# Kernel optimization log

Measured on AMD Instinct MI355X. Metric: run time of the kernel, lower is better.

The kernel has to match this reference:

```python
import jax, jax.numpy as jnp
import numpy as np

N, E, IN, H = 20000, 50000, 32, 64


def _lin_init(k, fan_in, shape):
    b = 1.0 / np.sqrt(fan_in)
    return jax.random.uniform(k, shape, jnp.float32, -b, b)


def setup_inputs() -> dict:
    key = jax.random.key(0)
    ks = jax.random.split(key, 16)
    inp = {
        "x": jax.random.normal(ks[0], (N, IN), jnp.float32),
        "edge_index": jax.random.randint(ks[1], (2, E), 0, N, dtype=jnp.int32),
        "edge_attr": jax.random.normal(ks[2], (E, 1, 2), jnp.float32),
        # layer 0: edge MLP 2->H->IN*H, root [IN,H], bias [H]
        "w1_0": _lin_init(ks[3], 2, (2, H)),
        "b1_0": _lin_init(ks[4], 2, (H,)),
        "w2_0": _lin_init(ks[5], H, (H, IN * H)),
        "b2_0": _lin_init(ks[6], H, (IN * H,)),
        "root_0": _lin_init(ks[7], IN, (IN, H)),
        "bias_0": _lin_init(ks[8], IN, (H,)),
        # layer 1: edge MLP 2->H->H*H, root [H,H], bias [H]
        "w1_1": _lin_init(ks[9], 2, (2, H)),
        "b1_1": _lin_init(ks[10], 2, (H,)),
        "w2_1": _lin_init(ks[11], H, (H, H * H)),
        "b2_1": _lin_init(ks[12], H, (H * H,)),
        "root_1": _lin_init(ks[13], H, (H, H)),
        "bias_1": _lin_init(ks[14], H, (H,)),
    }
    return inp


def _nnconv(x, src, dst, ea, w1, b1, w2, b2, root, bias, in_c, out_c):
    # per-edge weight matrices from edge-attr MLP: [E, in_c*out_c]
    h = jax.nn.relu(ea @ w1 + b1) @ w2 + b2
    W = h.reshape(-1, in_c, out_c)                     # [E, in, out]
    msg = jnp.einsum('ei,eio->eo', x[src], W)          # gather + per-edge matmul
    agg = jax.ops.segment_sum(msg, dst, num_segments=x.shape[0])  # scatter-add
    return agg + x @ root + bias                       # add aggr (PyG NNConv, aggr='add')


def reference(x, edge_index, edge_attr,
              w1_0, b1_0, w2_0, b2_0, root_0, bias_0,
              w1_1, b1_1, w2_1, b2_1, root_1, bias_1):
    src, dst = edge_index[0], edge_index[1]
    ea = edge_attr.reshape(edge_attr.shape[0], 2)      # [E, 2]
    x = jax.nn.relu(_nnconv(x, src, dst, ea, w1_0, b1_0, w2_0, b2_0, root_0, bias_0, IN, H))
    x = jax.nn.relu(_nnconv(x, src, dst, ea, w1_1, b1_1, w2_1, b2_1, root_1, bias_1, H, H))
    return x
```

## Files before the change

### kernel.cpp

```cpp
#include <hip/hip_runtime.h>

typedef _Float16 v8h __attribute__((ext_vector_type(8)));
typedef float v16f __attribute__((ext_vector_type(16)));

#define NBF0 (68 * 2 * 2 * 512)
#define NBF1 (68 * 4 * 2 * 512)

__global__ void prep_bf_both(const float* __restrict__ w2_0, const float* __restrict__ b2_0,
                             _Float16* __restrict__ BF0,
                             const float* __restrict__ w2_1, const float* __restrict__ b2_1,
                             _Float16* __restrict__ BF1) {
    int idx = blockIdx.x * 256 + threadIdx.x;
    if (idx < NBF0) {
        int rel = idx;
        int j = rel & 7, lane = (rel >> 3) & 63, f = rel >> 9;
        int nf = f & 1, kk16 = f >> 1;
        int k = kk16 * 16 + (lane >> 5) * 8 + j;
        int ko = k >> 5, i = k & 31;
        int o = nf * 32 + (lane & 31);
        float v = (ko < 64) ? w2_0[ko * (32 * 64) + i * 64 + o]
                : (ko == 64 ? b2_0[i * 64 + o] : 0.f);
        BF0[rel] = (_Float16)v;
    } else if (idx < NBF0 + NBF1) {
        int rel = idx - NBF0;
        int j = rel & 7, lane = (rel >> 3) & 63, f = rel >> 9;
        int nf = f & 1, kk16 = f >> 1;
        int k = kk16 * 16 + (lane >> 5) * 8 + j;
        int ko = k >> 6, i = k & 63;
        int o = nf * 32 + (lane & 31);
        float v = (ko < 64) ? w2_1[ko * (64 * 64) + i * 64 + o]
                : (ko == 64 ? b2_1[i * 64 + o] : 0.f);
        BF1[rel] = (_Float16)v;
    }
}

__global__ void node_root_cvt(const float* __restrict__ x, const float* __restrict__ root,
                              const float* __restrict__ bias, float* __restrict__ agg,
                              _Float16* __restrict__ xb, int N) {
    int idx = blockIdx.x * 256 + threadIdx.x;
    if (idx >= N * 64) return;
    int n = idx >> 6, o = idx & 63;
    float s = bias[o];
    const float* xr = x + (size_t)n * 32;
    #pragma unroll 8
    for (int i = 0; i < 32; ++i) s += xr[i] * root[i * 64 + o];
    agg[idx] = s;
    if (o < 32) xb[n * 32 + o] = (_Float16)xr[o];
}

__global__ void mid_kernel(const float* __restrict__ agg0, const float* __restrict__ root1,
                           const float* __restrict__ bias1, _Float16* __restrict__ x1b,
                           float* __restrict__ agg1, int N) {
    int idx = blockIdx.x * 256 + threadIdx.x;
    if (idx >= N * 64) return;
    int n = idx >> 6, o = idx & 63;
    const float* ar = agg0 + (size_t)n * 64;
    float s = bias1[o];
    #pragma unroll 8
    for (int i = 0; i < 64; ++i) s += fmaxf(ar[i], 0.f) * root1[i * 64 + o];
    agg1[idx] = s;
    x1b[idx] = (_Float16)fmaxf(agg0[idx], 0.f);
}

__global__ void final_relu(const float* __restrict__ agg1, float* __restrict__ out, int n) {
    int idx = blockIdx.x * 256 + threadIdx.x;
    if (idx < n) out[idx] = fmaxf(agg1[idx], 0.f);
}

template<int IN_C>
__global__ __launch_bounds__(256) __attribute__((amdgpu_waves_per_eu(3, 3)))
void edge_gemm(const float* __restrict__ ea,
               const float* __restrict__ w1, const float* __restrict__ b1v,
               const _Float16* __restrict__ xb, const _Float16* __restrict__ BF,
               const int* __restrict__ srcI, const int* __restrict__ dstI,
               float* __restrict__ agg, int E) {
    constexpr int PH  = IN_C / 16;
    constexpr int CPR = IN_C / 8;

    __shared__ __align__(16) _Float16 sh_x[64][IN_C];
    __shared__ _Float16 sh_r1[64][70];
    __shared__ float buf[64][65];
    __shared__ int sh_dst[64];

    int tid = threadIdx.x;
    int ebase = blockIdx.x * 64;
    int valid = E - ebase; if (valid > 64) valid = 64;

    if (tid < 64) {
        sh_dst[tid] = (tid < valid) ? dstI[ebase + tid] : 0;
        sh_r1[tid][64] = (_Float16)1.f;
        #pragma unroll
        for (int c = 65; c < 70; ++c) sh_r1[tid][c] = (_Float16)0.f;
    }
    for (int i = tid; i < 64 * 64; i += 256) {
        int e = i >> 6, j = i & 63;
        int ge = (e < valid) ? (ebase + e) : ebase;
        float a0 = ea[ge * 2], a1 = ea[ge * 2 + 1];
        sh_r1[e][j] = (_Float16)fmaxf(a0 * w1[j] + a1 * w1[64 + j] + b1v[j], 0.f);
    }
    for (int i = tid; i < 64 * CPR; i += 256) {
        int r = i / CPR, c = i - r * CPR;
        int sidx = (r < valid) ? srcI[ebase + r] : 0;
        *(uint4*)&sh_x[r][c * 8] = *(const uint4*)(xb + (size_t)sidx * IN_C + (size_t)c * 8);
    }
    __syncthreads();

    int wv = tid >> 6, lane = tid & 63, ln = lane & 31, g2 = lane >> 5;
    int nf = wv & 1, kh = wv >> 1;

    v8h xs0[PH], xs1[PH];
    #pragma unroll
    for (int p = 0; p < PH; ++p) {
        xs0[p] = *(const v8h*)&sh_x[ln][p * 16 + g2 * 8];
        xs1[p] = *(const v8h*)&sh_x[ln + 32][p * 16 + g2 * 8];
    }

    v16f acc0 = {0,0,0,0,0,0,0,0,0,0,0,0,0,0,0,0};
    v16f acc1 = acc0;

    const uint4* bp = (const uint4*)BF + (size_t)nf * 64 + lane;
    int kb = kh * 33;

    uint4 pb0[PH], pb1[PH], pb2[PH];
    auto LD = [&](uint4 (&d)[PH], int ko) {
        #pragma unroll
        for (int p = 0; p < PH; ++p) d[p] = bp[(size_t)(ko * PH + p) * 128];
    };
    auto FM = [&](uint4 (&d)[PH], int ko) {
        _Float16 sv0 = sh_r1[ln][ko];
        _Float16 sv1 = sh_r1[ln + 32][ko];
        #pragma unroll
        for (int p = 0; p < PH; ++p) {
            v8h bb; __builtin_memcpy(&bb, &d[p], 16);
            v8h a0 = xs0[p] * sv0;
            v8h a1 = xs1[p] * sv1;
            acc0 = __builtin_amdgcn_mfma_f32_32x32x16_f16(a0, bb, acc0, 0, 0, 0);
            acc1 = __builtin_amdgcn_mfma_f32_32x32x16_f16(a1, bb, acc1, 0, 0, 0);
        }
    };

    LD(pb0, kb);
    LD(pb1, kb + 1);
    #pragma unroll 1
    for (int t = 0; t < 11; ++t) {
        int base = kb + 3 * t;
        LD(pb2, base + 2);
        FM(pb0, base);
        LD(pb0, base + 3);
        FM(pb1, base + 1);
        LD(pb1, base + 4);
        FM(pb2, base + 2);
    }

    int colb = nf * 32 + ln;
    if (kh == 1) {
        #pragma unroll
        for (int r = 0; r < 16; ++r) {
            int row = 4 * g2 + (r & 3) + 8 * (r >> 2);
            buf[row][colb]      = acc0[r];
            buf[row + 32][colb] = acc1[r];
        }
    }
    __syncthreads();
    if (kh == 0) {
        #pragma unroll
        for (int r = 0; r < 16; ++r) {
            int row = 4 * g2 + (r & 3) + 8 * (r >> 2);
            if (row < valid)
                atomicAdd(&agg[(size_t)sh_dst[row] * 64 + colb], acc0[r] + buf[row][colb]);
            int row1 = row + 32;
            if (row1 < valid)
                atomicAdd(&agg[(size_t)sh_dst[row1] * 64 + colb], acc1[r] + buf[row1][colb]);
        }
    }
}

extern "C" void kernel_launch(void* const* d_in, const int* in_sizes, int n_in,
                              void* d_out, int out_size, void* d_ws, size_t ws_size,
                              hipStream_t stream) {
    const float* x      = (const float*)d_in[0];
    const int*   ei     = (const int*)d_in[1];
    const float* ea     = (const float*)d_in[2];
    const float* w1_0   = (const float*)d_in[3];
    const float* b1_0   = (const float*)d_in[4];
    const float* w2_0   = (const float*)d_in[5];
    const float* b2_0   = (const float*)d_in[6];
    const float* root_0 = (const float*)d_in[7];
    const float* bias_0 = (const float*)d_in[8];
    const float* w1_1   = (const float*)d_in[9];
    const float* b1_1   = (const float*)d_in[10];
    const float* w2_1   = (const float*)d_in[11];
    const float* b2_1   = (const float*)d_in[12];
    const float* root_1 = (const float*)d_in[13];
    const float* bias_1 = (const float*)d_in[14];
    float* out = (float*)d_out;

    int N = in_sizes[0] / 32;
    int E = in_sizes[1] / 2;
    const int* srcI = ei;
    const int* dstI = ei + E;

    char* ws = (char*)d_ws;
    size_t off = 0;
    auto carve = [&](size_t bytes) {
        void* p = ws + off;
        off += (bytes + 255) & ~(size_t)255;
        return p;
    };
    _Float16* BF0  = (_Float16*)carve((size_t)NBF0 * 2);
    _Float16* BF1  = (_Float16*)carve((size_t)NBF1 * 2);
    _Float16* XB0  = (_Float16*)carve((size_t)N * 32 * 2);
    _Float16* X1B  = (_Float16*)carve((size_t)N * 64 * 2);
    float*    AGG0 = (float*)carve((size_t)N * 64 * 4);
    float*    AGG1 = (float*)carve((size_t)N * 64 * 4);

    int tbf = NBF0 + NBF1;
    prep_bf_both<<<(tbf + 255) / 256, 256, 0, stream>>>(w2_0, b2_0, BF0, w2_1, b2_1, BF1);
    node_root_cvt<<<(N * 64 + 255) / 256, 256, 0, stream>>>(x, root_0, bias_0, AGG0, XB0, N);

    int gblocks = (E + 63) / 64;
    edge_gemm<32><<<gblocks, 256, 0, stream>>>(ea, w1_0, b1_0, XB0, BF0, srcI, dstI, AGG0, E);

    mid_kernel<<<(N * 64 + 255) / 256, 256, 0, stream>>>(AGG0, root_1, bias_1, X1B, AGG1, N);

    edge_gemm<64><<<gblocks, 256, 0, stream>>>(ea, w1_1, b1_1, X1B, BF1, srcI, dstI, AGG1, E);

    final_relu<<<(N * 64 + 255) / 256, 256, 0, stream>>>(AGG1, out, N * 64);
}
```

Measured before the change: 191.7 us.

## Split K dimension four ways per wave and reduce via shared-memory atomics

Each of the four waves now computes the full 64x64 output tile over a quarter of the K range (17 outer steps), reusing each A fragment across both N halves with four accumulators. Partial results are combined with LDS atomicAdd into a zeroed buffer, then all threads issue coalesced global atomics. This removes the redundant A-operand scaling per N half and the manual triple-buffered prefetch pipeline. In exchange it costs extra accumulator registers, LDS atomic contention, and the loss of explicit load/compute overlap.

```diff
diff --git a/kernel.cpp b/kernel.cpp
--- a/kernel.cpp
+++ b/kernel.cpp
@@ -78,7 +78,7 @@
     constexpr int CPR = IN_C / 8;
 
     __shared__ __align__(16) _Float16 sh_x[64][IN_C];
-    __shared__ _Float16 sh_r1[64][70];
+    __shared__ _Float16 sh_r1[64][72];
     __shared__ float buf[64][65];
     __shared__ int sh_dst[64];
 
@@ -90,7 +90,7 @@
         sh_dst[tid] = (tid < valid) ? dstI[ebase + tid] : 0;
         sh_r1[tid][64] = (_Float16)1.f;
         #pragma unroll
-        for (int c = 65; c < 70; ++c) sh_r1[tid][c] = (_Float16)0.f;
+        for (int c = 65; c < 72; ++c) sh_r1[tid][c] = (_Float16)0.f;
     }
     for (int i = tid; i < 64 * 64; i += 256) {
         int e = i >> 6, j = i & 63;
@@ -103,10 +103,13 @@
         int sidx = (r < valid) ? srcI[ebase + r] : 0;
         *(uint4*)&sh_x[r][c * 8] = *(const uint4*)(xb + (size_t)sidx * IN_C + (size_t)c * 8);
     }
+    {
+        float* bf = &buf[0][0];
+        for (int i = tid; i < 64 * 65; i += 256) bf[i] = 0.f;
+    }
     __syncthreads();
 
     int wv = tid >> 6, lane = tid & 63, ln = lane & 31, g2 = lane >> 5;
-    int nf = wv & 1, kh = wv >> 1;
 
     v8h xs0[PH], xs1[PH];
     #pragma unroll
@@ -115,63 +118,51 @@
         xs1[p] = *(const v8h*)&sh_x[ln + 32][p * 16 + g2 * 8];
     }
 
-    v16f acc0 = {0,0,0,0,0,0,0,0,0,0,0,0,0,0,0,0};
-    v16f acc1 = acc0;
-
-    const uint4* bp = (const uint4*)BF + (size_t)nf * 64 + lane;
-    int kb = kh * 33;
-
-    uint4 pb0[PH], pb1[PH], pb2[PH];
-    auto LD = [&](uint4 (&d)[PH], int ko) {
-        #pragma unroll
-        for (int p = 0; p < PH; ++p) d[p] = bp[(size_t)(ko * PH + p) * 128];
-    };
-    auto FM = [&](uint4 (&d)[PH], int ko) {
+    v16f acc00 = {0,0,0,0,0,0,0,0,0,0,0,0,0,0,0,0};
+    v16f acc01 = acc00, acc10 = acc00, acc11 = acc00;
+
+    const uint4* bp = (const uint4*)BF + lane;
+    int kb = wv * 17;
+
+    for (int ko = kb; ko < kb + 17; ++ko) {
+        uint4 b0[PH], b1[PH];
+        #pragma unroll
+        for (int p = 0; p < PH; ++p) {
+            size_t f2 = (size_t)(ko * PH + p) * 2;
+            b0[p] = bp[f2 * 64];
+            b1[p] = bp[(f2 + 1) * 64];
+        }
         _Float16 sv0 = sh_r1[ln][ko];
         _Float16 sv1 = sh_r1[ln + 32][ko];
         #pragma unroll
         for (int p = 0; p < PH; ++p) {
-            v8h bb; __builtin_memcpy(&bb, &d[p], 16);
+            v8h bb0; __builtin_memcpy(&bb0, &b0[p], 16);
+            v8h bb1; __builtin_memcpy(&bb1, &b1[p], 16);
             v8h a0 = xs0[p] * sv0;
             v8h a1 = xs1[p] * sv1;
-            acc0 = __builtin_amdgcn_mfma_f32_32x32x16_f16(a0, bb, acc0, 0, 0, 0);
-            acc1 = __builtin_amdgcn_mfma_f32_32x32x16_f16(a1, bb, acc1, 0, 0, 0);
+            acc00 = __builtin_amdgcn_mfma_f32_32x32x16_f16(a0, bb0, acc00, 0, 0, 0);
+            acc01 = __builtin_amdgcn_mfma_f32_32x32x16_f16(a0, bb1, acc01, 0, 0, 0);
+            acc10 = __builtin_amdgcn_mfma_f32_32x32x16_f16(a1, bb0, acc10, 0, 0, 0);
+            acc11 = __builtin_amdgcn_mfma_f32_32x32x16_f16(a1, bb1, acc11, 0, 0, 0);
+        }
+    }
+
+    auto emit = [&](const v16f& c, int mf, int nf) {
+        int col = nf * 32 + ln;
+        #pragma unroll
+        for (int r = 0; r < 16; ++r) {
+            int row = mf * 32 + 4 * g2 + (r & 3) + 8 * (r >> 2);
+            atomicAdd(&buf[row][col], c[r]);
         }
     };
-
-    LD(pb0, kb);
-    LD(pb1, kb + 1);
-    #pragma unroll 1
-    for (int t = 0; t < 11; ++t) {
-        int base = kb + 3 * t;
-        LD(pb2, base + 2);
-        FM(pb0, base);
-        LD(pb0, base + 3);
-        FM(pb1, base + 1);
-        LD(pb1, base + 4);
-        FM(pb2, base + 2);
-    }
-
-    int colb = nf * 32 + ln;
-    if (kh == 1) {
-        #pragma unroll
-        for (int r = 0; r < 16; ++r) {
-            int row = 4 * g2 + (r & 3) + 8 * (r >> 2);
-            buf[row][colb]      = acc0[r];
-            buf[row + 32][colb] = acc1[r];
-        }
-    }
+    emit(acc00, 0, 0); emit(acc01, 0, 1);
+    emit(acc10, 1, 0); emit(acc11, 1, 1);
     __syncthreads();
-    if (kh == 0) {
-        #pragma unroll
-        for (int r = 0; r < 16; ++r) {
-            int row = 4 * g2 + (r & 3) + 8 * (r >> 2);
-            if (row < valid)
-                atomicAdd(&agg[(size_t)sh_dst[row] * 64 + colb], acc0[r] + buf[row][colb]);
-            int row1 = row + 32;
-            if (row1 < valid)
-                atomicAdd(&agg[(size_t)sh_dst[row1] * 64 + colb], acc1[r] + buf[row1][colb]);
-        }
+
+    for (int t = tid; t < 64 * 64; t += 256) {
+        int row = t >> 6, col = t & 63;
+        if (row < valid)
+            atomicAdd(&agg[(size_t)sh_dst[row] * 64 + col], buf[row][col]);
     }
 }
 
```

New measurement: 347.2 us. 81.1% more time.

## Stage edge-MLP weight fragments in LDS via async loads, split K across grid

Applied to the files above, without the earlier changes.

Each block now covers 128 edges instead of 64. The K dimension (hidden units plus the bias row) is split across a second grid dimension, so every block handles 34 K-steps for all 128 edges. Weight fragments are copied into a double-buffered LDS area with global_load_lds and shared by the two 64-edge wave groups, where before each wave read them straight from global memory. This halves the weight traffic per edge and drops the in-block cross-wave reduction buffer. The costs are a __syncthreads on every K-step, twice as many atomicAdds (one per K-half) and the removed waves_per_eu hint.

```diff
diff --git a/kernel.cpp b/kernel.cpp
--- a/kernel.cpp
+++ b/kernel.cpp
@@ -68,110 +68,96 @@
 }
 
 template<int IN_C>
-__global__ __launch_bounds__(256) __attribute__((amdgpu_waves_per_eu(3, 3)))
+__global__ __launch_bounds__(256)
 void edge_gemm(const float* __restrict__ ea,
                const float* __restrict__ w1, const float* __restrict__ b1v,
                const _Float16* __restrict__ xb, const _Float16* __restrict__ BF,
                const int* __restrict__ srcI, const int* __restrict__ dstI,
                float* __restrict__ agg, int E) {
-    constexpr int PH  = IN_C / 16;
-    constexpr int CPR = IN_C / 8;
-
-    __shared__ __align__(16) _Float16 sh_x[64][IN_C];
-    __shared__ _Float16 sh_r1[64][70];
-    __shared__ float buf[64][65];
-    __shared__ int sh_dst[64];
+    constexpr int PH    = IN_C / 16;
+    constexpr int NB_FR = PH * 2;
+    constexpr int CPR   = IN_C / 8;
+    constexpr int KO_B  = 34;
+
+    __shared__ __align__(16) _Float16 sh_b[2][NB_FR * 512];
+    __shared__ __align__(16) _Float16 sh_x[128][IN_C];
+    __shared__ _Float16 sh_r1[128][36];
+    __shared__ int sh_dst[128];
 
     int tid = threadIdx.x;
-    int ebase = blockIdx.x * 64;
-    int valid = E - ebase; if (valid > 64) valid = 64;
-
-    if (tid < 64) {
-        sh_dst[tid] = (tid < valid) ? dstI[ebase + tid] : 0;
-        sh_r1[tid][64] = (_Float16)1.f;
-        #pragma unroll
-        for (int c = 65; c < 70; ++c) sh_r1[tid][c] = (_Float16)0.f;
-    }
-    for (int i = tid; i < 64 * 64; i += 256) {
-        int e = i >> 6, j = i & 63;
+    int ebase = blockIdx.x * 128;
+    int kb = blockIdx.y * KO_B;
+    int valid = E - ebase; if (valid > 128) valid = 128;
+
+    if (tid < 128) sh_dst[tid] = (tid < valid) ? dstI[ebase + tid] : 0;
+
+    for (int i = tid; i < 128 * 36; i += 256) {
+        int e = i / 36, jj = i - e * 36;
+        int j = kb + jj;
         int ge = (e < valid) ? (ebase + e) : ebase;
-        float a0 = ea[ge * 2], a1 = ea[ge * 2 + 1];
-        sh_r1[e][j] = (_Float16)fmaxf(a0 * w1[j] + a1 * w1[64 + j] + b1v[j], 0.f);
-    }
-    for (int i = tid; i < 64 * CPR; i += 256) {
+        float v;
+        if (j < 64)       v = fmaxf(ea[ge * 2] * w1[j] + ea[ge * 2 + 1] * w1[64 + j] + b1v[j], 0.f);
+        else if (j == 64) v = 1.f;
+        else              v = 0.f;
+        sh_r1[e][jj] = (_Float16)v;
+    }
+    for (int i = tid; i < 128 * CPR; i += 256) {
         int r = i / CPR, c = i - r * CPR;
         int sidx = (r < valid) ? srcI[ebase + r] : 0;
         *(uint4*)&sh_x[r][c * 8] = *(const uint4*)(xb + (size_t)sidx * IN_C + (size_t)c * 8);
     }
+
+    int wv = tid >> 6, lane = tid & 63, ln = lane & 31, g2 = lane >> 5;
+    int nf = wv & 1, eg = wv >> 1;
+
+    auto stage = [&](int c, int buf) {
+        const _Float16* g = BF + (size_t)(kb + c) * (NB_FR * 512);
+        for (int q = wv; q < NB_FR; q += 4) {
+            __builtin_amdgcn_global_load_lds(
+                (const __attribute__((address_space(1))) void*)(g + q * 512 + lane * 8),
+                (__attribute__((address_space(3))) void*)(&sh_b[buf][q * 512]),
+                16, 0, 0);
+        }
+    };
+
+    stage(0, 0);
     __syncthreads();
-
-    int wv = tid >> 6, lane = tid & 63, ln = lane & 31, g2 = lane >> 5;
-    int nf = wv & 1, kh = wv >> 1;
 
     v8h xs0[PH], xs1[PH];
     #pragma unroll
     for (int p = 0; p < PH; ++p) {
-        xs0[p] = *(const v8h*)&sh_x[ln][p * 16 + g2 * 8];
-        xs1[p] = *(const v8h*)&sh_x[ln + 32][p * 16 + g2 * 8];
+        xs0[p] = *(const v8h*)&sh_x[eg * 64 + ln][p * 16 + g2 * 8];
+        xs1[p] = *(const v8h*)&sh_x[eg * 64 + 32 + ln][p * 16 + g2 * 8];
     }
 
     v16f acc0 = {0,0,0,0,0,0,0,0,0,0,0,0,0,0,0,0};
     v16f acc1 = acc0;
 
-    const uint4* bp = (const uint4*)BF + (size_t)nf * 64 + lane;
-    int kb = kh * 33;
-
-    uint4 pb0[PH], pb1[PH], pb2[PH];
-    auto LD = [&](uint4 (&d)[PH], int ko) {
-        #pragma unroll
-        for (int p = 0; p < PH; ++p) d[p] = bp[(size_t)(ko * PH + p) * 128];
-    };
-    auto FM = [&](uint4 (&d)[PH], int ko) {
-        _Float16 sv0 = sh_r1[ln][ko];
-        _Float16 sv1 = sh_r1[ln + 32][ko];
+    for (int c = 0; c < KO_B; ++c) {
+        if (c + 1 < KO_B) stage(c + 1, (c + 1) & 1);
+        const _Float16* bb = sh_b[c & 1];
+        _Float16 sv0 = sh_r1[eg * 64 + ln][c];
+        _Float16 sv1 = sh_r1[eg * 64 + 32 + ln][c];
         #pragma unroll
         for (int p = 0; p < PH; ++p) {
-            v8h bb; __builtin_memcpy(&bb, &d[p], 16);
+            v8h bf = *(const v8h*)(bb + (p * 2 + nf) * 512 + lane * 8);
             v8h a0 = xs0[p] * sv0;
             v8h a1 = xs1[p] * sv1;
-            acc0 = __builtin_amdgcn_mfma_f32_32x32x16_f16(a0, bb, acc0, 0, 0, 0);
-            acc1 = __builtin_amdgcn_mfma_f32_32x32x16_f16(a1, bb, acc1, 0, 0, 0);
+            acc0 = __builtin_amdgcn_mfma_f32_32x32x16_f16(a0, bf, acc0, 0, 0, 0);
+            acc1 = __builtin_amdgcn_mfma_f32_32x32x16_f16(a1, bf, acc1, 0, 0, 0);
         }
-    };
-
-    LD(pb0, kb);
-    LD(pb1, kb + 1);
-    #pragma unroll 1
-    for (int t = 0; t < 11; ++t) {
-        int base = kb + 3 * t;
-        LD(pb2, base + 2);
-        FM(pb0, base);
-        LD(pb0, base + 3);
-        FM(pb1, base + 1);
-        LD(pb1, base + 4);
-        FM(pb2, base + 2);
+        __syncthreads();
     }
 
     int colb = nf * 32 + ln;
-    if (kh == 1) {
-        #pragma unroll
-        for (int r = 0; r < 16; ++r) {
-            int row = 4 * g2 + (r & 3) + 8 * (r >> 2);
-            buf[row][colb]      = acc0[r];
-            buf[row + 32][colb] = acc1[r];
-        }
-    }
-    __syncthreads();
-    if (kh == 0) {
-        #pragma unroll
-        for (int r = 0; r < 16; ++r) {
-            int row = 4 * g2 + (r & 3) + 8 * (r >> 2);
-            if (row < valid)
-                atomicAdd(&agg[(size_t)sh_dst[row] * 64 + colb], acc0[r] + buf[row][colb]);
-            int row1 = row + 32;
-            if (row1 < valid)
-                atomicAdd(&agg[(size_t)sh_dst[row1] * 64 + colb], acc1[r] + buf[row1][colb]);
-        }
+    #pragma unroll
+    for (int r = 0; r < 16; ++r) {
+        int row = eg * 64 + 4 * g2 + (r & 3) + 8 * (r >> 2);
+        if (row < valid)
+            atomicAdd(&agg[(size_t)sh_dst[row] * 64 + colb], acc0[r]);
+        int row1 = row + 32;
+        if (row1 < valid)
+            atomicAdd(&agg[(size_t)sh_dst[row1] * 64 + colb], acc1[r]);
     }
 }
 
@@ -218,12 +204,12 @@
     prep_bf_both<<<(tbf + 255) / 256, 256, 0, stream>>>(w2_0, b2_0, BF0, w2_1, b2_1, BF1);
     node_root_cvt<<<(N * 64 + 255) / 256, 256, 0, stream>>>(x, root_0, bias_0, AGG0, XB0, N);
 
-    int gblocks = (E + 63) / 64;
-    edge_gemm<32><<<gblocks, 256, 0, stream>>>(ea, w1_0, b1_0, XB0, BF0, srcI, dstI, AGG0, E);
+    dim3 ggrid((E + 127) / 128, 2);
+    edge_gemm<32><<<ggrid, 256, 0, stream>>>(ea, w1_0, b1_0, XB0, BF0, srcI, dstI, AGG0, E);
 
     mid_kernel<<<(N * 64 + 255) / 256, 256, 0, stream>>>(AGG0, root_1, bias_1, X1B, AGG1, N);
 
-    edge_gemm<64><<<gblocks, 256, 0, stream>>>(ea, w1_1, b1_1, X1B, BF1, srcI, dstI, AGG1, E);
+    edge_gemm<64><<<ggrid, 256, 0, stream>>>(ea, w1_1, b1_1, X1B, BF1, srcI, dstI, AGG1, E);
 
     final_relu<<<(N * 64 + 255) / 256, 256, 0, stream>>>(AGG1, out, N * 64);
 }
```

After: 230.7 us. +20.4%, slower.
